# Kernel tuning notes

Hardware: AMD Instinct MI355X
Metric: run time of the kernel (lower is better)

Reference implementation:

```python
import jax, jax.numpy as jnp
import numpy as np

MASK_W = 1.0
KPT_W = 0.5

SOBEL_X = jnp.array([[-1.0, 0.0, 1.0], [-2.0, 0.0, 2.0], [-1.0, 0.0, 1.0]], jnp.float32).reshape(1, 1, 3, 3)
SOBEL_Y = jnp.array([[-1.0, -2.0, -1.0], [0.0, 0.0, 0.0], [1.0, 2.0, 1.0]], jnp.float32).reshape(1, 1, 3, 3)
BOX = jnp.ones((1, 1, 3, 3), jnp.float32)


def conv3x3(x, k):
    # x: [N,1,H,W]; torch F.conv2d is cross-correlation, same as lax conv
    return jax.lax.conv_general_dilated(
        x, k, window_strides=(1, 1), padding=[(1, 1), (1, 1)],
        dimension_numbers=('NCHW', 'OIHW', 'NCHW'))


def sobel_edge(mask):
    ex = conv3x3(mask, SOBEL_X)
    ey = conv3x3(mask, SOBEL_Y)
    return jnp.sqrt(ex * ex + ey * ey)


def grid_sample_bilinear_zeros(img, grid):
    # img: [H,W]; grid: [K,2] in [-1,1], (x,y) order; align_corners=False, zero padding
    H, W = img.shape
    x = (grid[:, 0] + 1.0) * (W * 0.5) - 0.5
    y = (grid[:, 1] + 1.0) * (H * 0.5) - 0.5
    x0 = jnp.floor(x).astype(jnp.int32)
    y0 = jnp.floor(y).astype(jnp.int32)
    x1 = x0 + 1
    y1 = y0 + 1
    wx1 = x - x0.astype(x.dtype)
    wx0 = 1.0 - wx1
    wy1 = y - y0.astype(y.dtype)
    wy0 = 1.0 - wy1

    def gather(ix, iy):
        valid = (ix >= 0) & (ix < W) & (iy >= 0) & (iy < H)
        v = img[jnp.clip(iy, 0, H - 1), jnp.clip(ix, 0, W - 1)]
        return jnp.where(valid, v, 0.0)

    return (wx0 * wy0 * gather(x0, y0) + wx1 * wy0 * gather(x1, y0)
            + wx0 * wy1 * gather(x0, y1) + wx1 * wy1 * gather(x1, y1))


def setup_inputs() -> dict:
    key = jax.random.key(0)
    k1, k2, k3, k4 = jax.random.split(key, 4)
    return {
        'pred_keypoints': jax.random.uniform(k1, (1024, 2), jnp.float32),
        'target_keypoints': jax.random.uniform(k2, (1024, 2), jnp.float32),
        'pred_seg': jax.random.uniform(k3, (1, 1, 4096, 4096), jnp.float32),
        'target_seg': jax.random.uniform(k4, (1, 1, 4096, 4096), jnp.float32),
    }


def reference(pred_keypoints, target_keypoints, pred_seg, target_seg):
    target_edge = sobel_edge(target_seg)
    pred_edge = sobel_edge(pred_seg)
    edge_loss = jnp.mean((pred_edge - target_edge) ** 2)
    distance_map = conv3x3(pred_edge, BOX)  # [1,1,H,W]
    kd = grid_sample_bilinear_zeros(distance_map[0, 0], pred_keypoints)  # [K]
    constraint_loss = jnp.mean(kd)
    return MASK_W * edge_loss + KPT_W * constraint_loss
```

## Files before the change

### kernel.cpp

```cpp
#include <hip/hip_runtime.h>

#define H 4096
#define W 4096
#define TH 32
#define BX 256
#define GX 4
#define GY (H / TH)
#define NEDGE (GX * GY)
#define NKPB 16

#define MASK_W 1.0f
#define KPT_W 0.5f

struct RowData { float v0, v1, v2, v3, lf, rf; };
struct Prep { float dx0, dx1, dx2, dx3, s0, s1, s2, s3; };

__device__ __forceinline__ RowData loadrow(const float* __restrict__ img, int r, int c) {
    RowData rd;
    if ((unsigned)r < (unsigned)H) {
        const float* p = img + (size_t)r * W + c;
        float4 v = *(const float4*)p;
        rd.v0 = v.x; rd.v1 = v.y; rd.v2 = v.z; rd.v3 = v.w;
        rd.lf = (c == 0) ? 0.f : p[-1];
        rd.rf = (c + 4 == W) ? 0.f : p[4];
    } else {
        rd.v0 = rd.v1 = rd.v2 = rd.v3 = rd.lf = rd.rf = 0.f;
    }
    return rd;
}

__device__ __forceinline__ Prep prep(const RowData& rd) {
    Prep o;
    o.dx0 = rd.v1 - rd.lf;
    o.dx1 = rd.v2 - rd.v0;
    o.dx2 = rd.v3 - rd.v1;
    o.dx3 = rd.rf - rd.v2;
    o.s0 = __fmaf_rn(2.f, rd.v0, rd.lf + rd.v1);
    o.s1 = __fmaf_rn(2.f, rd.v1, rd.v0 + rd.v2);
    o.s2 = __fmaf_rn(2.f, rd.v2, rd.v1 + rd.v3);
    o.s3 = __fmaf_rn(2.f, rd.v3, rd.v2 + rd.rf);
    return o;
}

__device__ __forceinline__ float edge1(float dxA, float dxB, float dxC, float sA, float sC) {
    float ex = dxA + __fmaf_rn(2.f, dxB, dxC);
    float ey = sC - sA;
    return sqrtf(__fmaf_rn(ex, ex, ey * ey));
}

__global__ __launch_bounds__(BX) void fused_kernel(const float* __restrict__ pred,
                                                   const float* __restrict__ targ,
                                                   const float* __restrict__ kp,
                                                   float* __restrict__ ws) {
    int bid = blockIdx.x;

    if (bid < NEDGE) {
        int gx = bid & (GX - 1);
        int gy = bid >> 2;
        int c = gx * (BX * 4) + threadIdx.x * 4;
        int r0 = gy * TH;

        Prep pA = prep(loadrow(pred, r0 - 1, c));
        Prep pB = prep(loadrow(pred, r0,     c));
        Prep tA = prep(loadrow(targ, r0 - 1, c));
        Prep tB = prep(loadrow(targ, r0,     c));
        RowData pn = loadrow(pred, r0 + 1, c);
        RowData tn = loadrow(targ, r0 + 1, c);

        float acc = 0.f;
        for (int r = r0; r < r0 + TH; ++r) {
            RowData pc = pn, tc = tn;
            if (r < r0 + TH - 1) {
                pn = loadrow(pred, r + 2, c);
                tn = loadrow(targ, r + 2, c);
            }
            Prep pC = prep(pc);
            Prep tC = prep(tc);

            float pe, te, d;
            pe = edge1(pA.dx0, pB.dx0, pC.dx0, pA.s0, pC.s0);
            te = edge1(tA.dx0, tB.dx0, tC.dx0, tA.s0, tC.s0);
            d = pe - te; acc = __fmaf_rn(d, d, acc);
            pe = edge1(pA.dx1, pB.dx1, pC.dx1, pA.s1, pC.s1);
            te = edge1(tA.dx1, tB.dx1, tC.dx1, tA.s1, tC.s1);
            d = pe - te; acc = __fmaf_rn(d, d, acc);
            pe = edge1(pA.dx2, pB.dx2, pC.dx2, pA.s2, pC.s2);
            te = edge1(tA.dx2, tB.dx2, tC.dx2, tA.s2, tC.s2);
            d = pe - te; acc = __fmaf_rn(d, d, acc);
            pe = edge1(pA.dx3, pB.dx3, pC.dx3, pA.s3, pC.s3);
            te = edge1(tA.dx3, tB.dx3, tC.dx3, tA.s3, tC.s3);
            d = pe - te; acc = __fmaf_rn(d, d, acc);

            pA = pB; pB = pC;
            tA = tB; tB = tC;
        }

        #pragma unroll
        for (int m = 32; m; m >>= 1) acc += __shfl_xor(acc, m);

        __shared__ float wsum[BX / 64];
        if ((threadIdx.x & 63) == 0) wsum[threadIdx.x >> 6] = acc;
        __syncthreads();
        if (threadIdx.x == 0) {
            float s = 0.f;
            #pragma unroll
            for (int i = 0; i < BX / 64; ++i) s += wsum[i];
            ws[bid] = s;
        }
    } else {
        int t = threadIdx.x;
        if (t >= 64) return;
        int k = (bid - NEDGE) * 64 + t;

        float gx = kp[2 * k];
        float gy = kp[2 * k + 1];
        float x = (gx + 1.f) * (W * 0.5f) - 0.5f;
        float y = (gy + 1.f) * (H * 0.5f) - 0.5f;
        float fx0 = floorf(x), fy0 = floorf(y);
        int x0 = (int)fx0, y0 = (int)fy0;
        int x1 = x0 + 1, y1 = y0 + 1;
        float wx1 = x - fx0, wx0 = 1.f - wx1;
        float wy1 = y - fy0, wy0 = 1.f - wy1;

        float sg[6][6];
        #pragma unroll
        for (int i = 0; i < 6; ++i) {
            int rr = y0 - 2 + i;
            #pragma unroll
            for (int j = 0; j < 6; ++j) {
                int cc = x0 - 2 + j;
                bool ok = (rr >= 0) & (rr < H) & (cc >= 0) & (cc < W);
                sg[i][j] = ok ? pred[(size_t)rr * W + cc] : 0.f;
            }
        }

        float e[4][4];
        #pragma unroll
        for (int i = 0; i < 4; ++i) {
            int rr = y0 - 1 + i;
            #pragma unroll
            for (int j = 0; j < 4; ++j) {
                int cc = x0 - 1 + j;
                if (rr < 0 || rr >= H || cc < 0 || cc >= W) { e[i][j] = 0.f; continue; }
                float ex = (sg[i][j + 2] - sg[i][j])
                         + 2.f * (sg[i + 1][j + 2] - sg[i + 1][j])
                         + (sg[i + 2][j + 2] - sg[i + 2][j]);
                float ey = (sg[i + 2][j] + 2.f * sg[i + 2][j + 1] + sg[i + 2][j + 2])
                         - (sg[i][j] + 2.f * sg[i][j + 1] + sg[i][j + 2]);
                e[i][j] = sqrtf(__fmaf_rn(ex, ex, ey * ey));
            }
        }

        float dmap[2][2];
        #pragma unroll
        for (int a = 0; a < 2; ++a) {
            #pragma unroll
            for (int b = 0; b < 2; ++b) {
                float s = 0.f;
                #pragma unroll
                for (int i = 0; i < 3; ++i)
                    #pragma unroll
                    for (int j = 0; j < 3; ++j) s += e[a + i][b + j];
                dmap[a][b] = s;
            }
        }

        bool vx0 = (x0 >= 0) & (x0 < W), vx1 = (x1 >= 0) & (x1 < W);
        bool vy0 = (y0 >= 0) & (y0 < H), vy1 = (y1 >= 0) & (y1 < H);
        float v00 = (vx0 & vy0) ? dmap[0][0] : 0.f;
        float v01 = (vx1 & vy0) ? dmap[0][1] : 0.f;
        float v10 = (vx0 & vy1) ? dmap[1][0] : 0.f;
        float v11 = (vx1 & vy1) ? dmap[1][1] : 0.f;
        float kd = wx0 * wy0 * v00 + wx1 * wy0 * v01
                 + wx0 * wy1 * v10 + wx1 * wy1 * v11;

        #pragma unroll
        for (int m = 32; m; m >>= 1) kd += __shfl_xor(kd, m);
        if (t == 0) ws[NEDGE + (bid - NEDGE)] = kd;
    }
}

__global__ __launch_bounds__(64) void final_kernel(const float* __restrict__ ws,
                                                   float* __restrict__ out) {
    int t = threadIdx.x;
    float es = 0.f;
    #pragma unroll
    for (int i = 0; i < NEDGE / 64; ++i) es += ws[t + i * 64];
    float ks = (t < NKPB) ? ws[NEDGE + t] : 0.f;

    #pragma unroll
    for (int m = 32; m; m >>= 1) {
        es += __shfl_xor(es, m);
        ks += __shfl_xor(ks, m);
    }
    if (t == 0) {
        float edge_loss = es * (1.f / ((float)H * (float)W));
        float constraint_loss = ks * (1.f / 1024.f);
        out[0] = MASK_W * edge_loss + KPT_W * constraint_loss;
    }
}

extern "C" void kernel_launch(void* const* d_in, const int* in_sizes, int n_in,
                              void* d_out, int out_size, void* d_ws, size_t ws_size,
                              hipStream_t stream) {
    const float* kp   = (const float*)d_in[0];
    const float* pred = (const float*)d_in[2];
    const float* targ = (const float*)d_in[3];
    float* out = (float*)d_out;
    float* ws  = (float*)d_ws;

    fused_kernel<<<NEDGE + NKPB, BX, 0, stream>>>(pred, targ, kp, ws);
    final_kernel<<<1, 64, 0, stream>>>(ws, out);
}
```

Before: 154.7 us.

## Share halo columns via lane shuffles, halve row tile, use hardware sqrt

New measurement: 168.9 us. +9.2%, slower.

```diff
diff --git a/kernel.cpp b/kernel.cpp
--- a/kernel.cpp
+++ b/kernel.cpp
@@ -2,7 +2,7 @@
 
 #define H 4096
 #define W 4096
-#define TH 32
+#define TH 16
 #define BX 256
 #define GX 4
 #define GY (H / TH)
@@ -15,16 +15,26 @@
 struct RowData { float v0, v1, v2, v3, lf, rf; };
 struct Prep { float dx0, dx1, dx2, dx3, s0, s1, s2, s3; };
 
-__device__ __forceinline__ RowData loadrow(const float* __restrict__ img, int r, int c) {
+__device__ __forceinline__ float fast_sqrt(float x) {
+    return __builtin_amdgcn_sqrtf(x);
+}
+
+__device__ __forceinline__ RowData loadrow_fast(const float* __restrict__ rowptr,
+                                                int c, bool rvalid) {
+    float4 v;
+    if (rvalid) v = *(const float4*)rowptr;
+    else        v = make_float4(0.f, 0.f, 0.f, 0.f);
     RowData rd;
-    if ((unsigned)r < (unsigned)H) {
-        const float* p = img + (size_t)r * W + c;
-        float4 v = *(const float4*)p;
-        rd.v0 = v.x; rd.v1 = v.y; rd.v2 = v.z; rd.v3 = v.w;
-        rd.lf = (c == 0) ? 0.f : p[-1];
-        rd.rf = (c + 4 == W) ? 0.f : p[4];
-    } else {
-        rd.v0 = rd.v1 = rd.v2 = rd.v3 = rd.lf = rd.rf = 0.f;
+    rd.v0 = v.x; rd.v1 = v.y; rd.v2 = v.z; rd.v3 = v.w;
+    rd.lf = __shfl_up(v.w, 1);
+    rd.rf = __shfl_down(v.x, 1);
+    int lane = threadIdx.x & 63;
+    if (lane == 0 || lane == 63) {
+        bool left = (lane == 0);
+        bool ok = rvalid && (left ? (c > 0) : (c + 4 < W));
+        const float* q = left ? (rowptr - 1) : (rowptr + 4);
+        float h = ok ? *q : 0.f;
+        if (left) rd.lf = h; else rd.rf = h;
     }
     return rd;
 }
@@ -45,7 +55,7 @@
 __device__ __forceinline__ float edge1(float dxA, float dxB, float dxC, float sA, float sC) {
     float ex = dxA + __fmaf_rn(2.f, dxB, dxC);
     float ey = sC - sA;
-    return sqrtf(__fmaf_rn(ex, ex, ey * ey));
+    return fast_sqrt(__fmaf_rn(ex, ex, ey * ey));
 }
 
 __global__ __launch_bounds__(BX) void fused_kernel(const float* __restrict__ pred,
@@ -57,22 +67,30 @@
     if (bid < NEDGE) {
         int gx = bid & (GX - 1);
         int gy = bid >> 2;
-        int c = gx * (BX * 4) + threadIdx.x * 4;
+        int c  = gx * (BX * 4) + threadIdx.x * 4;
         int r0 = gy * TH;
 
-        Prep pA = prep(loadrow(pred, r0 - 1, c));
-        Prep pB = prep(loadrow(pred, r0,     c));
-        Prep tA = prep(loadrow(targ, r0 - 1, c));
-        Prep tB = prep(loadrow(targ, r0,     c));
-        RowData pn = loadrow(pred, r0 + 1, c);
-        RowData tn = loadrow(targ, r0 + 1, c);
+        const float* prow = pred + (size_t)r0 * W + c;
+        const float* trow = targ + (size_t)r0 * W + c;
+
+        Prep pA = prep(loadrow_fast(prow - W, c, r0 > 0));
+        Prep pB = prep(loadrow_fast(prow,     c, true));
+        Prep tA = prep(loadrow_fast(trow - W, c, r0 > 0));
+        Prep tB = prep(loadrow_fast(trow,     c, true));
+        RowData pn = loadrow_fast(prow + W, c, true);
+        RowData tn = loadrow_fast(trow + W, c, true);
+        prow += 2 * (size_t)W;
+        trow += 2 * (size_t)W;
 
         float acc = 0.f;
-        for (int r = r0; r < r0 + TH; ++r) {
+        #pragma unroll 4
+        for (int i = 0; i < TH; ++i) {
             RowData pc = pn, tc = tn;
-            if (r < r0 + TH - 1) {
-                pn = loadrow(pred, r + 2, c);
-                tn = loadrow(targ, r + 2, c);
+            if (i < TH - 1) {
+                bool nvalid = (r0 + i + 2) < H;
+                pn = loadrow_fast(prow, c, nvalid);
+                tn = loadrow_fast(trow, c, nvalid);
+                prow += W; trow += W;
             }
             Prep pC = prep(pc);
             Prep tC = prep(tc);
@@ -147,7 +165,7 @@
                          + (sg[i + 2][j + 2] - sg[i + 2][j]);
                 float ey = (sg[i + 2][j] + 2.f * sg[i + 2][j + 1] + sg[i + 2][j + 2])
                          - (sg[i][j] + 2.f * sg[i][j + 1] + sg[i][j + 2]);
-                e[i][j] = sqrtf(__fmaf_rn(ex, ex, ey * ey));
+                e[i][j] = fast_sqrt(__fmaf_rn(ex, ex, ey * ey));
             }
         }
 
@@ -180,12 +198,12 @@
     }
 }
 
-__global__ __launch_bounds__(64) void final_kernel(const float* __restrict__ ws,
-                                                   float* __restrict__ out) {
+__global__ __launch_bounds__(256) void final_kernel(const float* __restrict__ ws,
+                                                    float* __restrict__ out) {
     int t = threadIdx.x;
     float es = 0.f;
     #pragma unroll
-    for (int i = 0; i < NEDGE / 64; ++i) es += ws[t + i * 64];
+    for (int i = 0; i < NEDGE / 256; ++i) es += ws[t + i * 256];
     float ks = (t < NKPB) ? ws[NEDGE + t] : 0.f;
 
     #pragma unroll
@@ -193,9 +211,15 @@
         es += __shfl_xor(es, m);
         ks += __shfl_xor(ks, m);
     }
+    __shared__ float res[4], rks[4];
+    int wid = t >> 6;
+    if ((t & 63) == 0) { res[wid] = es; rks[wid] = ks; }
+    __syncthreads();
     if (t == 0) {
-        float edge_loss = es * (1.f / ((float)H * (float)W));
-        float constraint_loss = ks * (1.f / 1024.f);
+        float e2 = res[0] + res[1] + res[2] + res[3];
+        float k2 = rks[0] + rks[1] + rks[2] + rks[3];
+        float edge_loss = e2 * (1.f / ((float)H * (float)W));
+        float constraint_loss = k2 * (1.f / 1024.f);
         out[0] = MASK_W * edge_loss + KPT_W * constraint_loss;
     }
 }
@@ -210,5 +234,5 @@
     float* ws  = (float*)d_ws;
 
     fused_kernel<<<NEDGE + NKPB, BX, 0, stream>>>(pred, targ, kp, ws);
-    final_kernel<<<1, 64, 0, stream>>>(ws, out);
-}
+    final_kernel<<<1, 256, 0, stream>>>(ws, out);
+}
```
